# Kernel tuning notes

Measured on AMD Instinct MI355X. Metric: run time of the kernel, lower is better.

The kernel has to match this reference:

```python
import jax, jax.numpy as jnp
import numpy as np

B, S, E, H = 1, 8192, 1024, 16
D = E // H
SEG_LENS = [2048, 4096, 8192]
DILATIONS = [1, 2, 4]


def setup_inputs() -> dict:
    key = jax.random.key(0)
    k0, k1, k2 = jax.random.split(key, 3)
    sc_in = 1.0 / np.sqrt(E)
    return {
        "x": jax.random.normal(k0, (B, S, E), jnp.float32),
        "w_qkv": jax.random.normal(k1, (3 * E, E), jnp.float32) * sc_in,
        "b_qkv": jnp.zeros((3 * E,), jnp.float32),
        "w_out": jax.random.normal(k2, (E, E), jnp.float32) * sc_in,
        "b_out": jnp.zeros((E,), jnp.float32),
    }


def _sdpa(q, k, v):
    # q,k,v: [B,H,N,D]; standard scaled dot-product attention (non-causal)
    scale = 1.0 / np.sqrt(q.shape[-1])
    scores = jnp.einsum('bhqd,bhkd->bhqk', q, k) * scale
    probs = jax.nn.softmax(scores, axis=-1)
    return jnp.einsum('bhqk,bhkd->bhqd', probs, v)


def reference(x, w_qkv, b_qkv, w_out, b_out):
    # QKV projection: torch Linear is x @ W^T + b
    qkv = x @ w_qkv.T + b_qkv                       # [B,S,3E]
    qkv = qkv.reshape(B, S, 3, H, D).transpose(2, 0, 3, 1, 4)  # [3,B,H,S,D]
    q, k, v = qkv[0], qkv[1], qkv[2]

    seg_outputs = []
    for seg_len, dil in zip(SEG_LENS, DILATIONS):
        if seg_len > S:
            continue
        if dil > 1:
            n = min(seg_len, S // dil)
            pos = np.arange(0, n * dil, dil)        # strided dilated gather
        else:
            pos = np.arange(seg_len)                # leading segment
        o = _sdpa(q[:, :, pos], k[:, :, pos], v[:, :, pos])
        # scatter back to full length (zero elsewhere); also handles zero-padding
        full = jnp.zeros((B, H, S, D), x.dtype).at[:, :, pos, :].set(o)
        seg_outputs.append(full)

    if len(seg_outputs) == 0:
        out = jnp.zeros((B, H, S, D), x.dtype)
    else:
        out = seg_outputs[0]
        for so in seg_outputs[1:]:
            out = out + so
        out = out / len(seg_outputs)                # stack(...).mean(0)

    out = out.transpose(0, 2, 1, 3).reshape(B, S, E)
    return out @ w_out.T + b_out
```

## Files before the change

### kernel.cpp

```cpp
#include <hip/hip_runtime.h>


typedef __attribute__((ext_vector_type(8))) short bf16x8;
typedef __attribute__((ext_vector_type(4))) float f32x4;

#define MFMA(a, b, c) __builtin_amdgcn_mfma_f32_16x16x32_bf16((a), (b), (c), 0, 0, 0)

#if __has_builtin(__builtin_amdgcn_exp2f)
#define EXP2(x) __builtin_amdgcn_exp2f(x)
#else
#define EXP2(x) exp2f(x)
#endif

static __device__ __forceinline__ unsigned short f2bf(float f) {
  unsigned int u = __float_as_uint(f);
  unsigned int r = (u + 0x7FFFu + ((u >> 16) & 1u)) >> 16;
  return (unsigned short)r;
}

__global__ void cvt_f32_bf16(const float* __restrict__ in,
                             unsigned short* __restrict__ out, int n8) {
  int i = blockIdx.x * blockDim.x + threadIdx.x;
  if (i >= n8) return;
  const float4* p = (const float4*)in + (size_t)i * 2;
  float4 a = p[0];
  float4 b = p[1];
  union { bf16x8 v; unsigned short u[8]; } o;
  o.u[0] = f2bf(a.x); o.u[1] = f2bf(a.y); o.u[2] = f2bf(a.z); o.u[3] = f2bf(a.w);
  o.u[4] = f2bf(b.x); o.u[5] = f2bf(b.y); o.u[6] = f2bf(b.z); o.u[7] = f2bf(b.w);
  *((bf16x8*)out + i) = o.v;
}

template <int EPILOGUE>
__global__ __launch_bounds__(256, 2) void gemm_bt(
    const unsigned short* __restrict__ A, const unsigned short* __restrict__ B,
    const float* __restrict__ bias, void* __restrict__ Cout, int N, int K) {
  __shared__ unsigned short At[128 * 32];
  __shared__ unsigned short Bt[128 * 32];
  const int tid = threadIdx.x;
  const int wave = tid >> 6, lane = tid & 63;
  const int quad = lane >> 4, lc = lane & 15;
  const int wm = (wave >> 1) * 64, wn = (wave & 1) * 64;
  const int m0 = blockIdx.x * 128, n0 = blockIdx.y * 128;

  f32x4 acc[4][4] = {};

  for (int k0 = 0; k0 < K; k0 += 32) {
    __syncthreads();
#pragma unroll
    for (int issue = 0; issue < 2; ++issue) {
      const int cbase = issue * 256 + wave * 64;
      const int c = cbase + lane;
      const int row = c >> 2, col8 = (c & 3) * 8;
      __builtin_amdgcn_global_load_lds(
          (const __attribute__((address_space(1))) void*)&A[(size_t)(m0 + row) * K + k0 + col8],
          (__attribute__((address_space(3))) void*)&At[cbase * 8], 16, 0, 0);
      __builtin_amdgcn_global_load_lds(
          (const __attribute__((address_space(1))) void*)&B[(size_t)(n0 + row) * K + k0 + col8],
          (__attribute__((address_space(3))) void*)&Bt[cbase * 8], 16, 0, 0);
    }
    __syncthreads();
    bf16x8 af[4], bfr[4];
#pragma unroll
    for (int t = 0; t < 4; ++t)
      af[t] = *(const bf16x8*)&At[(wm + t * 16 + lc) * 32 + quad * 8];
#pragma unroll
    for (int t = 0; t < 4; ++t)
      bfr[t] = *(const bf16x8*)&Bt[(wn + t * 16 + lc) * 32 + quad * 8];
#pragma unroll
    for (int i = 0; i < 4; ++i)
#pragma unroll
      for (int j = 0; j < 4; ++j)
        acc[i][j] = MFMA(af[i], bfr[j], acc[i][j]);
  }

#pragma unroll
  for (int i = 0; i < 4; ++i) {
#pragma unroll
    for (int j = 0; j < 4; ++j) {
      const int gcol = n0 + wn + j * 16 + lc;
      const float bs = bias[gcol];
#pragma unroll
      for (int r = 0; r < 4; ++r) {
        const int grow = m0 + wm + i * 16 + quad * 4 + r;
        const float v = acc[i][j][r] + bs;
        if (EPILOGUE == 0) {
          const int which = gcol >> 10, rem = gcol & 1023;
          const int hh = rem >> 6, d = rem & 63;
          const float vs = (which == 0) ? v * 0.18033688f : v;
          ((unsigned short*)Cout)[(((size_t)(which * 16 + hh)) * 8192 + grow) * 64 + d] = f2bf(vs);
        } else {
          ((float*)Cout)[(size_t)grow * N + gcol] = v;
        }
      }
    }
  }
}

__global__ void transpose_v(const unsigned short* __restrict__ v,
                            unsigned short* __restrict__ vt1,
                            unsigned short* __restrict__ vt2,
                            unsigned short* __restrict__ vt3) {
  __shared__ unsigned short Tt[64 * 72];
  const int tid = threadIdx.x;
  const int h = blockIdx.y;
  const int bx = blockIdx.x;
  const unsigned short* src = v + (size_t)h * 8192 * 64;
  unsigned short* dst;
  int dil, Nk, t0;
  if (bx < 32)      { dst = vt1; dil = 1; Nk = 2048; t0 = bx; }
  else if (bx < 96) { dst = vt2; dil = 2; Nk = 4096; t0 = bx - 32; }
  else              { dst = vt3; dil = 4; Nk = 2048; t0 = bx - 96; }
  dst += (size_t)h * 64 * Nk;
  const int j0 = t0 * 64;
#pragma unroll
  for (int it = 0; it < 2; ++it) {
    const int slot = tid + it * 256;
    const int jj = slot >> 3, c8 = (slot & 7) * 8;
    *(bf16x8*)&Tt[jj * 72 + c8] =
        *(const bf16x8*)&src[(size_t)(j0 + jj) * dil * 64 + c8];
  }
  __syncthreads();
  const int d = tid >> 2, pg = (tid & 3) * 16;
  union { bf16x8 v2[2]; unsigned short u[16]; } ob;
#pragma unroll
  for (int t = 0; t < 16; ++t) {
    const int pos = pg + t;
    const int w = pos & 31;
    const int jj = (pos & 32) | (((w >> 2) & 1) * 16 + (w >> 3) * 4 + (w & 3));
    ob.u[t] = Tt[jj * 72 + d];
  }
  *(bf16x8*)&dst[(size_t)d * Nk + j0 + pg] = ob.v2[0];
  *(bf16x8*)&dst[(size_t)d * Nk + j0 + pg + 8] = ob.v2[1];
}

__global__ __launch_bounds__(256, 3) void flash_all(
    const unsigned short* __restrict__ qkvb,
    const unsigned short* __restrict__ vt1, float* __restrict__ o1,
    const unsigned short* __restrict__ vt2, float* __restrict__ o2a,
    float* __restrict__ o2b, float* __restrict__ l2a, float* __restrict__ l2b,
    const unsigned short* __restrict__ vt3, float* __restrict__ o3) {
  __shared__ unsigned short Smem[2 * 64 * 64];
  unsigned short* Kt = Smem;
  unsigned short* Vt = Smem + 64 * 64;

  const int bx = blockIdx.x;
  const int i = bx / 3;
  const int r = bx - 3 * i;
  int z, h, qt, kb0;
  const unsigned short* vt;
  float* o;
  float* lout = nullptr;
  if (r < 2) {
    z = 1; h = i >> 4; qt = i & 15; kb0 = r * 2048;
    vt = vt2; o = (r == 0) ? o2a : o2b; lout = (r == 0) ? l2a : l2b;
  } else if (i < 128) {
    z = 0; h = i >> 3; qt = i & 7; kb0 = 0; vt = vt1; o = o1;
  } else {
    const int j = i - 128;
    z = 2; h = j >> 3; qt = j & 7; kb0 = 0; vt = vt3; o = o3;
  }
  const int Nk = (z == 1) ? 4096 : 2048;
  const int kbEnd = kb0 + 2048;
  const int dil = 1 << z;
  const bool split = (r < 2);

  const int tid = threadIdx.x;
  const int wave = tid >> 6, lane = tid & 63;
  const int quad = lane >> 4, lc = lane & 15;

  const unsigned short* qh = qkvb + (size_t)h * 8192 * 64;
  const unsigned short* kh = qkvb + (size_t)(16 + h) * 8192 * 64;
  const unsigned short* vh = vt + (size_t)h * 64 * Nk;

  bf16x8 qf[4][2];
#pragma unroll
  for (int mb = 0; mb < 4; ++mb) {
    const size_t qrow = (size_t)(qt * 256 + wave * 64 + mb * 16 + lc) * dil;
    qf[mb][0] = *(const bf16x8*)&qh[qrow * 64 + quad * 8];
    qf[mb][1] = *(const bf16x8*)&qh[qrow * 64 + quad * 8 + 32];
  }

  union { bf16x8 v; unsigned short u[8]; } one_u;
#pragma unroll
  for (int t = 0; t < 8; ++t) one_u.u[t] = 0x3F80;
  const bf16x8 vone = one_u.v;

  f32x4 oacc[4][4] = {};
  f32x4 lacc[4] = {};

  const int srow = tid >> 3, scol = tid & 7;
  const int swz = (scol ^ (srow & 7)) * 8;

  bf16x8 kg0 = *(const bf16x8*)&kh[(size_t)((kb0 + srow) * dil) * 64 + scol * 8];
  bf16x8 kg1 = *(const bf16x8*)&kh[(size_t)((kb0 + srow + 32) * dil) * 64 + scol * 8];
  bf16x8 vg0 = *(const bf16x8*)&vh[(size_t)srow * Nk + kb0 + scol * 8];
  bf16x8 vg1 = *(const bf16x8*)&vh[(size_t)(srow + 32) * Nk + kb0 + scol * 8];

  for (int kb = kb0; kb < kbEnd; kb += 64) {
    __syncthreads();
    *(bf16x8*)&Kt[srow * 64 + swz] = kg0;
    *(bf16x8*)&Kt[(srow + 32) * 64 + swz] = kg1;
    *(bf16x8*)&Vt[srow * 64 + swz] = vg0;
    *(bf16x8*)&Vt[(srow + 32) * 64 + swz] = vg1;
    __syncthreads();

    if (kb + 64 < kbEnd) {
      const int nk = kb + 64;
      kg0 = *(const bf16x8*)&kh[(size_t)((nk + srow) * dil) * 64 + scol * 8];
      kg1 = *(const bf16x8*)&kh[(size_t)((nk + srow + 32) * dil) * 64 + scol * 8];
      vg0 = *(const bf16x8*)&vh[(size_t)srow * Nk + nk + scol * 8];
      vg1 = *(const bf16x8*)&vh[(size_t)(srow + 32) * Nk + nk + scol * 8];
    }

#pragma unroll
    for (int ks = 0; ks < 2; ++ks) {
      f32x4 st[2][4];
#pragma unroll
      for (int t = 0; t < 2; ++t) {
        const int row = (ks * 2 + t) * 16 + lc;
        const bf16x8 ka0 = *(const bf16x8*)&Kt[row * 64 + ((quad ^ (lc & 7)) * 8)];
        const bf16x8 ka1 = *(const bf16x8*)&Kt[row * 64 + (((4 + quad) ^ (lc & 7)) * 8)];
#pragma unroll
        for (int mb = 0; mb < 4; ++mb) {
          f32x4 zz = {};
          zz = MFMA(ka0, qf[mb][0], zz);
          st[t][mb] = MFMA(ka1, qf[mb][1], zz);
        }
      }

      bf16x8 pb[4];
#pragma unroll
      for (int mb = 0; mb < 4; ++mb) {
        union { bf16x8 v; unsigned int u[4]; } pu;
#pragma unroll
        for (int t = 0; t < 2; ++t) {
          const unsigned int a0 = __float_as_uint(EXP2(st[t][mb][0])) + 0x8000u;
          const unsigned int a1 = __float_as_uint(EXP2(st[t][mb][1])) + 0x8000u;
          const unsigned int a2 = __float_as_uint(EXP2(st[t][mb][2])) + 0x8000u;
          const unsigned int a3 = __float_as_uint(EXP2(st[t][mb][3])) + 0x8000u;
          pu.u[t * 2 + 0] = __builtin_amdgcn_perm(a1, a0, 0x07060302u);
          pu.u[t * 2 + 1] = __builtin_amdgcn_perm(a3, a2, 0x07060302u);
        }
        pb[mb] = pu.v;
      }

#pragma unroll
      for (int nb = 0; nb < 4; ++nb) {
        const int vrow = nb * 16 + lc;
        const bf16x8 va = *(const bf16x8*)&Vt[vrow * 64 + (((ks * 4 + quad) ^ (lc & 7)) * 8)];
#pragma unroll
        for (int mb = 0; mb < 4; ++mb)
          oacc[mb][nb] = MFMA(va, pb[mb], oacc[mb][nb]);
      }
#pragma unroll
      for (int mb = 0; mb < 4; ++mb) lacc[mb] = MFMA(vone, pb[mb], lacc[mb]);
    }
  }

  __syncthreads();
  float* W = (float*)Smem + wave * 16 * 64;
  const int g = lane >> 2, s4 = lane & 3;
#pragma unroll
  for (int mb = 0; mb < 4; ++mb) {
    const float inv = split ? 1.0f : 1.0f / (3.0f * lacc[mb][0]);
    if (split && quad == 0)
      lout[(size_t)h * 4096 + qt * 256 + wave * 64 + mb * 16 + lc] = lacc[mb][0];
#pragma unroll
    for (int nb = 0; nb < 4; ++nb) {
      const int c = nb * 4 + quad;
      const int cs = (c & 8) | ((c & 7) ^ (lc & 7));
      f32x4 val = oacc[mb][nb];
      val *= inv;
      *(f32x4*)&W[lc * 64 + cs * 4] = val;
    }
    const size_t base = (size_t)(qt * 256 + wave * 64 + mb * 16 + g) * 1024 +
                        (size_t)h * 64 + s4 * 16;
#pragma unroll
    for (int c2 = 0; c2 < 4; ++c2) {
      const int c = s4 * 4 + c2;
      const int cs = (c & 8) | ((c & 7) ^ (g & 7));
      *(float4*)&o[base + c2 * 4] = *(const float4*)&W[g * 64 + cs * 4];
    }
  }
}

__global__ void combine(const float* __restrict__ o1,
                        const float* __restrict__ o2a, const float* __restrict__ o2b,
                        const float* __restrict__ l2a, const float* __restrict__ l2b,
                        const float* __restrict__ o3,
                        unsigned short* __restrict__ a3b) {
  const int idx = blockIdx.x * 256 + threadIdx.x;
  const int s = idx >> 7, e = (idx & 127) * 8;
  float acc[8] = {};
  if (s < 2048) {
    const float* p = &o1[(size_t)s * 1024 + e];
#pragma unroll
    for (int t = 0; t < 8; ++t) acc[t] += p[t];
  }
  if (!(s & 1)) {
    const int j = s >> 1, hh = e >> 6;
    const float la = l2a[(size_t)hh * 4096 + j];
    const float lb = l2b[(size_t)hh * 4096 + j];
    const float w = 1.0f / (3.0f * (la + lb));
    const float* pa = &o2a[(size_t)j * 1024 + e];
    const float* pb = &o2b[(size_t)j * 1024 + e];
#pragma unroll
    for (int t = 0; t < 8; ++t) acc[t] += (pa[t] + pb[t]) * w;
  }
  if (!(s & 3)) {
    const float* p = &o3[(size_t)(s >> 2) * 1024 + e];
#pragma unroll
    for (int t = 0; t < 8; ++t) acc[t] += p[t];
  }
  union { bf16x8 v; unsigned short u[8]; } ob;
#pragma unroll
  for (int t = 0; t < 8; ++t) ob.u[t] = f2bf(acc[t]);
  *(bf16x8*)&a3b[(size_t)s * 1024 + e] = ob.v;
}

extern "C" void kernel_launch(void* const* d_in, const int* in_sizes, int n_in,
                              void* d_out, int out_size, void* d_ws, size_t ws_size,
                              hipStream_t stream) {
  const float* x     = (const float*)d_in[0];
  const float* w_qkv = (const float*)d_in[1];
  const float* b_qkv = (const float*)d_in[2];
  const float* w_out = (const float*)d_in[3];
  const float* b_out = (const float*)d_in[4];
  float* out = (float*)d_out;

  char* ws = (char*)d_ws;
  unsigned short* qkvb  = (unsigned short*)(ws);
  float*          o1    = (float*)(ws + 33554432);
  float*          o3    = (float*)(ws + 41943040);
  unsigned short* vt1   = (unsigned short*)(ws + 50331648);
  unsigned short* vt2   = (unsigned short*)(ws + 54525952);
  unsigned short* vt3   = (unsigned short*)(ws + 62914560);
  float*          o2a   = (float*)(ws + 67108864);
  unsigned short* wqkvb = (unsigned short*)(ws + 83886080);
  float*          l2a   = (float*)(ws + 83886080);
  float*          l2b   = (float*)(ws + 84148224);
  unsigned short* woutb = (unsigned short*)(ws + 90177536);
  unsigned short* xb    = (unsigned short*)(ws + 92274688);
  float*          o2b   = (float*)(ws + 92274688);
  unsigned short* a3b   = (unsigned short*)(ws + 50331648);

  cvt_f32_bf16<<<dim3(8388608 / 8 / 256), dim3(256), 0, stream>>>(x, xb, 8388608 / 8);
  cvt_f32_bf16<<<dim3(3145728 / 8 / 256), dim3(256), 0, stream>>>(w_qkv, wqkvb, 3145728 / 8);
  cvt_f32_bf16<<<dim3(1048576 / 8 / 256), dim3(256), 0, stream>>>(w_out, woutb, 1048576 / 8);

  gemm_bt<0><<<dim3(64, 24), dim3(256), 0, stream>>>(xb, wqkvb, b_qkv, qkvb, 3072, 1024);

  transpose_v<<<dim3(128, 16), dim3(256), 0, stream>>>(qkvb + (size_t)32 * 8192 * 64,
                                                       vt1, vt2, vt3);

  flash_all<<<dim3(768), dim3(256), 0, stream>>>(qkvb, vt1, o1, vt2, o2a, o2b,
                                                 l2a, l2b, vt3, o3);

  combine<<<dim3(4096), dim3(256), 0, stream>>>(o1, o2a, o2b, l2a, l2b, o3, a3b);

  gemm_bt<1><<<dim3(64, 8), dim3(256), 0, stream>>>(a3b, woutb, b_out, out, 1024, 1024);
}
```

Measured before the change: 349.4 us.

## Double-buffer flash K/V tiles, fuse conversions, vectorize GEMM epilogue, remap blocks

```diff
diff --git a/kernel.cpp b/kernel.cpp
--- a/kernel.cpp
+++ b/kernel.cpp
@@ -18,17 +18,24 @@
   return (unsigned short)r;
 }
 
-__global__ void cvt_f32_bf16(const float* __restrict__ in,
-                             unsigned short* __restrict__ out, int n8) {
-  int i = blockIdx.x * blockDim.x + threadIdx.x;
-  if (i >= n8) return;
-  const float4* p = (const float4*)in + (size_t)i * 2;
+__global__ void cvt_all(const float* __restrict__ x, const float* __restrict__ wq,
+                        const float* __restrict__ wo,
+                        unsigned short* __restrict__ xb,
+                        unsigned short* __restrict__ wqb,
+                        unsigned short* __restrict__ wob) {
+  int i = blockIdx.x * 256 + threadIdx.x;
+  const float* src;
+  unsigned short* dst;
+  if (i < 1048576) { src = x; dst = xb; }
+  else if (i < 1441792) { src = wq + (size_t)(i - 1048576) * 8 - 0; dst = wqb; i -= 1048576; src = wq; }
+  else { i -= 1441792; src = wo; dst = wob; }
+  const float4* p = (const float4*)src + (size_t)i * 2;
   float4 a = p[0];
   float4 b = p[1];
   union { bf16x8 v; unsigned short u[8]; } o;
   o.u[0] = f2bf(a.x); o.u[1] = f2bf(a.y); o.u[2] = f2bf(a.z); o.u[3] = f2bf(a.w);
   o.u[4] = f2bf(b.x); o.u[5] = f2bf(b.y); o.u[6] = f2bf(b.z); o.u[7] = f2bf(b.w);
-  *((bf16x8*)out + i) = o.v;
+  *((bf16x8*)dst + i) = o.v;
 }
 
 template <int EPILOGUE>
@@ -71,27 +78,42 @@
     for (int i = 0; i < 4; ++i)
 #pragma unroll
       for (int j = 0; j < 4; ++j)
-        acc[i][j] = MFMA(af[i], bfr[j], acc[i][j]);
-  }
-
-#pragma unroll
-  for (int i = 0; i < 4; ++i) {
-#pragma unroll
-    for (int j = 0; j < 4; ++j) {
-      const int gcol = n0 + wn + j * 16 + lc;
-      const float bs = bias[gcol];
-#pragma unroll
-      for (int r = 0; r < 4; ++r) {
-        const int grow = m0 + wm + i * 16 + quad * 4 + r;
-        const float v = acc[i][j][r] + bs;
-        if (EPILOGUE == 0) {
-          const int which = gcol >> 10, rem = gcol & 1023;
-          const int hh = rem >> 6, d = rem & 63;
-          const float vs = (which == 0) ? v * 0.18033688f : v;
-          ((unsigned short*)Cout)[(((size_t)(which * 16 + hh)) * 8192 + grow) * 64 + d] = f2bf(vs);
-        } else {
-          ((float*)Cout)[(size_t)grow * N + gcol] = v;
-        }
+        acc[i][j] = MFMA(bfr[j], af[i], acc[i][j]);
+  }
+
+#pragma unroll
+  for (int j = 0; j < 4; ++j) {
+    const int nc0 = n0 + wn + j * 16 + quad * 4;
+    const float4 bs4 = *(const float4*)&bias[nc0];
+    if (EPILOGUE == 0) {
+      const int which = nc0 >> 10, rem = nc0 & 1023;
+      const int hh = rem >> 6, d0 = rem & 63;
+      const float sc = (which == 0) ? 0.18033688f : 1.0f;
+      unsigned short* base =
+          (unsigned short*)Cout + ((size_t)(which * 16 + hh)) * 8192 * 64 + d0;
+#pragma unroll
+      for (int i = 0; i < 4; ++i) {
+        const int grow = m0 + wm + i * 16 + lc;
+        const unsigned int p0 = __float_as_uint((acc[i][j][0] + bs4.x) * sc) + 0x8000u;
+        const unsigned int p1 = __float_as_uint((acc[i][j][1] + bs4.y) * sc) + 0x8000u;
+        const unsigned int p2 = __float_as_uint((acc[i][j][2] + bs4.z) * sc) + 0x8000u;
+        const unsigned int p3 = __float_as_uint((acc[i][j][3] + bs4.w) * sc) + 0x8000u;
+        uint2 w;
+        w.x = __builtin_amdgcn_perm(p1, p0, 0x07060302u);
+        w.y = __builtin_amdgcn_perm(p3, p2, 0x07060302u);
+        *(uint2*)(base + (size_t)grow * 64) = w;
+      }
+    } else {
+      float* op = (float*)Cout;
+#pragma unroll
+      for (int i = 0; i < 4; ++i) {
+        const int grow = m0 + wm + i * 16 + lc;
+        float4 v;
+        v.x = acc[i][j][0] + bs4.x;
+        v.y = acc[i][j][1] + bs4.y;
+        v.z = acc[i][j][2] + bs4.z;
+        v.w = acc[i][j][3] + bs4.w;
+        *(float4*)&op[(size_t)grow * N + nc0] = v;
       }
     }
   }
@@ -140,30 +162,28 @@
     const unsigned short* __restrict__ vt2, float* __restrict__ o2a,
     float* __restrict__ o2b, float* __restrict__ l2a, float* __restrict__ l2b,
     const unsigned short* __restrict__ vt3, float* __restrict__ o3) {
-  __shared__ unsigned short Smem[2 * 64 * 64];
-  unsigned short* Kt = Smem;
-  unsigned short* Vt = Smem + 64 * 64;
+  __shared__ unsigned short Smem[2][2 * 64 * 64];
 
   const int bx = blockIdx.x;
-  const int i = bx / 3;
-  const int r = bx - 3 * i;
-  int z, h, qt, kb0;
+  const int x = bx & 7, g = bx >> 3;
+  const int h = x + ((g >= 48) ? 8 : 0);
+  const int gg = (g >= 48) ? g - 48 : g;
+  int z, qt, kb0;
   const unsigned short* vt;
   float* o;
   float* lout = nullptr;
-  if (r < 2) {
-    z = 1; h = i >> 4; qt = i & 15; kb0 = r * 2048;
-    vt = vt2; o = (r == 0) ? o2a : o2b; lout = (r == 0) ? l2a : l2b;
-  } else if (i < 128) {
-    z = 0; h = i >> 3; qt = i & 7; kb0 = 0; vt = vt1; o = o1;
+  bool split = false;
+  if (gg < 32) {
+    z = 1; qt = gg >> 1; kb0 = (gg & 1) * 2048; split = true;
+    vt = vt2; o = (gg & 1) ? o2b : o2a; lout = (gg & 1) ? l2b : l2a;
+  } else if (gg < 40) {
+    z = 0; qt = gg - 32; kb0 = 0; vt = vt1; o = o1;
   } else {
-    const int j = i - 128;
-    z = 2; h = j >> 3; qt = j & 7; kb0 = 0; vt = vt3; o = o3;
+    z = 2; qt = gg - 40; kb0 = 0; vt = vt3; o = o3;
   }
   const int Nk = (z == 1) ? 4096 : 2048;
   const int kbEnd = kb0 + 2048;
   const int dil = 1 << z;
-  const bool split = (r < 2);
 
   const int tid = threadIdx.x;
   const int wave = tid >> 6, lane = tid & 63;
@@ -196,22 +216,24 @@
   bf16x8 kg1 = *(const bf16x8*)&kh[(size_t)((kb0 + srow + 32) * dil) * 64 + scol * 8];
   bf16x8 vg0 = *(const bf16x8*)&vh[(size_t)srow * Nk + kb0 + scol * 8];
   bf16x8 vg1 = *(const bf16x8*)&vh[(size_t)(srow + 32) * Nk + kb0 + scol * 8];
-
+  *(bf16x8*)&Smem[0][srow * 64 + swz] = kg0;
+  *(bf16x8*)&Smem[0][(srow + 32) * 64 + swz] = kg1;
+  *(bf16x8*)&Smem[0][4096 + srow * 64 + swz] = vg0;
+  *(bf16x8*)&Smem[0][4096 + (srow + 32) * 64 + swz] = vg1;
+  __syncthreads();
+
+  int p = 0;
   for (int kb = kb0; kb < kbEnd; kb += 64) {
-    __syncthreads();
-    *(bf16x8*)&Kt[srow * 64 + swz] = kg0;
-    *(bf16x8*)&Kt[(srow + 32) * 64 + swz] = kg1;
-    *(bf16x8*)&Vt[srow * 64 + swz] = vg0;
-    *(bf16x8*)&Vt[(srow + 32) * 64 + swz] = vg1;
-    __syncthreads();
-
-    if (kb + 64 < kbEnd) {
+    const bool more = (kb + 64 < kbEnd);
+    if (more) {
       const int nk = kb + 64;
       kg0 = *(const bf16x8*)&kh[(size_t)((nk + srow) * dil) * 64 + scol * 8];
       kg1 = *(const bf16x8*)&kh[(size_t)((nk + srow + 32) * dil) * 64 + scol * 8];
       vg0 = *(const bf16x8*)&vh[(size_t)srow * Nk + nk + scol * 8];
       vg1 = *(const bf16x8*)&vh[(size_t)(srow + 32) * Nk + nk + scol * 8];
     }
+    const unsigned short* Kt = Smem[p];
+    const unsigned short* Vt = Smem[p] + 4096;
 
 #pragma unroll
     for (int ks = 0; ks < 2; ++ks) {
@@ -235,10 +257,10 @@
         union { bf16x8 v; unsigned int u[4]; } pu;
 #pragma unroll
         for (int t = 0; t < 2; ++t) {
-          const unsigned int a0 = __float_as_uint(EXP2(st[t][mb][0])) + 0x8000u;
-          const unsigned int a1 = __float_as_uint(EXP2(st[t][mb][1])) + 0x8000u;
-          const unsigned int a2 = __float_as_uint(EXP2(st[t][mb][2])) + 0x8000u;
-          const unsigned int a3 = __float_as_uint(EXP2(st[t][mb][3])) + 0x8000u;
+          const unsigned int a0 = __float_as_uint(EXP2(st[t][mb][0]));
+          const unsigned int a1 = __float_as_uint(EXP2(st[t][mb][1]));
+          const unsigned int a2 = __float_as_uint(EXP2(st[t][mb][2]));
+          const unsigned int a3 = __float_as_uint(EXP2(st[t][mb][3]));
           pu.u[t * 2 + 0] = __builtin_amdgcn_perm(a1, a0, 0x07060302u);
           pu.u[t * 2 + 1] = __builtin_amdgcn_perm(a3, a2, 0x07060302u);
         }
@@ -256,11 +278,19 @@
 #pragma unroll
       for (int mb = 0; mb < 4; ++mb) lacc[mb] = MFMA(vone, pb[mb], lacc[mb]);
     }
-  }
-
-  __syncthreads();
+
+    if (more) {
+      *(bf16x8*)&Smem[p ^ 1][srow * 64 + swz] = kg0;
+      *(bf16x8*)&Smem[p ^ 1][(srow + 32) * 64 + swz] = kg1;
+      *(bf16x8*)&Smem[p ^ 1][4096 + srow * 64 + swz] = vg0;
+      *(bf16x8*)&Smem[p ^ 1][4096 + (srow + 32) * 64 + swz] = vg1;
+    }
+    __syncthreads();
+    p ^= 1;
+  }
+
   float* W = (float*)Smem + wave * 16 * 64;
-  const int g = lane >> 2, s4 = lane & 3;
+  const int g2 = lane >> 2, s4 = lane & 3;
 #pragma unroll
   for (int mb = 0; mb < 4; ++mb) {
     const float inv = split ? 1.0f : 1.0f / (3.0f * lacc[mb][0]);
@@ -274,13 +304,13 @@
       val *= inv;
       *(f32x4*)&W[lc * 64 + cs * 4] = val;
     }
-    const size_t base = (size_t)(qt * 256 + wave * 64 + mb * 16 + g) * 1024 +
+    const size_t base = (size_t)(qt * 256 + wave * 64 + mb * 16 + g2) * 1024 +
                         (size_t)h * 64 + s4 * 16;
 #pragma unroll
     for (int c2 = 0; c2 < 4; ++c2) {
       const int c = s4 * 4 + c2;
-      const int cs = (c & 8) | ((c & 7) ^ (g & 7));
-      *(float4*)&o[base + c2 * 4] = *(const float4*)&W[g * 64 + cs * 4];
+      const int cs = (c & 8) | ((c & 7) ^ (g2 & 7));
+      *(float4*)&o[base + c2 * 4] = *(const float4*)&W[g2 * 64 + cs * 4];
     }
   }
 }
@@ -345,9 +375,7 @@
   float*          o2b   = (float*)(ws + 92274688);
   unsigned short* a3b   = (unsigned short*)(ws + 50331648);
 
-  cvt_f32_bf16<<<dim3(8388608 / 8 / 256), dim3(256), 0, stream>>>(x, xb, 8388608 / 8);
-  cvt_f32_bf16<<<dim3(3145728 / 8 / 256), dim3(256), 0, stream>>>(w_qkv, wqkvb, 3145728 / 8);
-  cvt_f32_bf16<<<dim3(1048576 / 8 / 256), dim3(256), 0, stream>>>(w_out, woutb, 1048576 / 8);
+  cvt_all<<<dim3(6144), dim3(256), 0, stream>>>(x, w_qkv, w_out, xb, wqkvb, woutb);
 
   gemm_bt<0><<<dim3(64, 24), dim3(256), 0, stream>>>(xb, wqkvb, b_qkv, qkvb, 3072, 1024);
 
```

Result: faster. 341.1 us (-2.4%).
